# Kernel optimization log

Hardware: AMD Instinct MI355X
Metric: run time of the kernel (lower is better)

## Reference

```python
import jax, jax.numpy as jnp
import numpy as np

B, CIN, CNECK, COUT = 8, 128, 128, 256
NV, NF = 10242, 20480  # icosphere level 5: nv = 10*4^5+2, nf = 20*4^5
EPS = 1e-5


def spmatmul(x, rows, cols, vals, m):
    # x: [..., N]; out[..., r] += vals[k] * x[..., cols[k]] for rows[k] == r
    g = x[..., cols] * vals
    return jnp.zeros(x.shape[:-1] + (m,), x.dtype).at[..., rows].add(g)


def conv1x1(x, w, b):
    # x: [B, Cin, N], w: [Cout, Cin], b: [Cout]
    return jnp.einsum('oi,bin->bon', w, x) + b[None, :, None]


def batchnorm1d(x, gamma, beta):
    # training-mode BN over (batch, spatial) per channel, biased variance
    mean = jnp.mean(x, axis=(0, 2), keepdims=True)
    var = jnp.var(x, axis=(0, 2), keepdims=True)
    xhat = (x - mean) * jax.lax.rsqrt(var + EPS)
    return gamma[None, :, None] * xhat + beta[None, :, None]


def setup_inputs() -> dict:
    key = jax.random.key(0)
    ks = jax.random.split(key, 16)

    def coo(k, nrows, per_row, ncols, scale):
        rows = jnp.repeat(jnp.arange(nrows, dtype=jnp.int32), per_row)
        cols = jax.random.randint(k, (nrows * per_row,), 0, ncols, dtype=jnp.int32)
        vals = jax.random.normal(jax.random.fold_in(k, 1), (nrows * per_row,), jnp.float32) * scale
        return rows, cols, vals

    Gr, Gc, Gv = coo(ks[0], 3 * NF, 3, NV, 0.5)
    Lr, Lc, Lv = coo(ks[1], NV, 7, NV, 0.3)
    Fr, Fc, Fv = coo(ks[2], NV, 6, NF, 1.0 / 6.0)

    def nrm(k, shape, scale=1.0):
        return jax.random.normal(k, shape, jnp.float32) * scale

    s_in = 1.0 / np.sqrt(CIN)
    s_nk = 1.0 / np.sqrt(CNECK)
    s_cf = 1.0 / np.sqrt(4 * CNECK)
    return {
        'x': nrm(ks[3], (B, CIN, NV)),
        'w1a': nrm(ks[4], (CNECK, CIN), s_in), 'b1a': nrm(ks[5], (CNECK,), s_in),
        'g1a': jnp.ones((CNECK,), jnp.float32), 'be1a': jnp.zeros((CNECK,), jnp.float32),
        'coeffs': nrm(ks[6], (CNECK * 4, CNECK), s_cf),
        'g2a': jnp.ones((CNECK,), jnp.float32), 'be2a': jnp.zeros((CNECK,), jnp.float32),
        'w3a': nrm(ks[7], (COUT, CNECK), s_nk), 'b3a': nrm(ks[8], (COUT,), s_nk),
        'g3a': jnp.ones((COUT,), jnp.float32), 'be3a': jnp.zeros((COUT,), jnp.float32),
        'w1b': nrm(ks[9], (COUT, CIN), s_in), 'b1b': nrm(ks[10], (COUT,), s_in),
        'g1b': jnp.ones((COUT,), jnp.float32), 'be1b': jnp.zeros((COUT,), jnp.float32),
        'G_vals': Gv, 'L_vals': Lv, 'F2V_vals': Fv,
        'EW': nrm(ks[11], (NF, 3)), 'NS': nrm(ks[12], (NF, 3)),
        'G_rows': Gr, 'G_cols': Gc,
        'L_rows': Lr, 'L_cols': Lc,
        'F2V_rows': Fr, 'F2V_cols': Fc,
    }


def mesh_conv(h, coeffs, G_rows, G_cols, G_vals, L_rows, L_cols, L_vals,
              F2V_rows, F2V_cols, F2V_vals, EW, NS):
    b, c, nv = h.shape
    # gradient on faces: [B,C,3*NF] -> [B,C,3,NF] -> [B,C,NF,3]
    grad_face = spmatmul(h, G_rows, G_cols, G_vals, 3 * NF)
    grad_face = grad_face.reshape(b, c, 3, NF).transpose(0, 1, 3, 2)
    laplacian = spmatmul(h, L_rows, L_cols, L_vals, NV)
    identity = h  # stride=1 => nv_prev == nv
    gf_ew = jnp.sum(grad_face * EW, axis=-1)  # [B,C,NF]
    gf_ns = jnp.sum(grad_face * NS, axis=-1)
    gv_ew = spmatmul(gf_ew, F2V_rows, F2V_cols, F2V_vals, NV)
    gv_ns = spmatmul(gf_ns, F2V_rows, F2V_cols, F2V_vals, NV)
    feat = jnp.stack([identity, laplacian, gv_ew, gv_ns], axis=-1)  # [B,C,NV,4]
    # [B,NV,C*4] @ [C*4,Cout] -> [B,Cout,NV]  (note: no bias added in original forward)
    out = jnp.matmul(feat.transpose(0, 2, 1, 3).reshape(b, nv, c * 4), coeffs)
    return out.transpose(0, 2, 1)


def reference(x, w1a, b1a, g1a, be1a, coeffs, g2a, be2a, w3a, b3a, g3a, be3a,
              w1b, b1b, g1b, be1b, G_vals, L_vals, F2V_vals, EW, NS,
              G_rows, G_cols, L_rows, L_cols, F2V_rows, F2V_cols):
    # shortcut branch: conv_1b -> bn_1b
    x2 = batchnorm1d(conv1x1(x, w1b, b1b), g1b, be1b)
    # main branch
    h = jax.nn.relu(batchnorm1d(conv1x1(x, w1a, b1a), g1a, be1a))
    h = mesh_conv(h, coeffs, G_rows, G_cols, G_vals, L_rows, L_cols, L_vals,
                  F2V_rows, F2V_cols, F2V_vals, EW, NS)
    h = jax.nn.relu(batchnorm1d(h, g2a, be2a))
    x1 = batchnorm1d(conv1x1(h, w3a, b3a), g3a, be3a)
    return jax.nn.relu(x1 + x2)
```

## Files before the change

### kernel.cpp

```cpp
#include <hip/hip_runtime.h>
#include <math.h>

#define BB   8
#define NVV  10242
#define NFF  20480
#define EPSBN 1e-5f
#define GRAM_BLOCKS 644

typedef __attribute__((ext_vector_type(8))) short bf16x8_t;
typedef __attribute__((ext_vector_type(4))) float f32x4_t;

__device__ inline float bf2f(ushort u) {
    union { uint i; float f; } v; v.i = ((uint)u) << 16; return v.f;
}
__device__ inline ushort f2bf(float f) {
    union { float f; uint i; } v; v.f = f;
    const uint r = v.i + 0x7fffu + ((v.i >> 16) & 1u);
    return (ushort)(r >> 16);
}
__device__ inline void unpack2(uint w, float& lo, float& hi) {
    union { uint i; float f; } a, b;
    a.i = w << 16; b.i = w & 0xffff0000u;
    lo = a.f; hi = b.f;
}
__device__ inline uint pack2(float lo, float hi) {
    return (uint)f2bf(lo) | ((uint)f2bf(hi) << 16);
}
__device__ inline void fma8(const uint4 hv, const float w, float s[8]) {
    float lo, hi;
    unpack2(hv.x, lo, hi); s[0] = fmaf(w, lo, s[0]); s[1] = fmaf(w, hi, s[1]);
    unpack2(hv.y, lo, hi); s[2] = fmaf(w, lo, s[2]); s[3] = fmaf(w, hi, s[3]);
    unpack2(hv.z, lo, hi); s[4] = fmaf(w, lo, s[4]); s[5] = fmaf(w, hi, s[5]);
    unpack2(hv.w, lo, hi); s[6] = fmaf(w, lo, s[6]); s[7] = fmaf(w, hi, s[7]);
}
__device__ inline uint4 pack8(const float s[8]) {
    uint4 p;
    p.x = pack2(s[0], s[1]); p.y = pack2(s[2], s[3]);
    p.z = pack2(s[4], s[5]); p.w = pack2(s[6], s[7]);
    return p;
}

__global__ __launch_bounds__(256)
void gram_kernel(const float* __restrict__ x, float* __restrict__ gramPart,
                 float* __restrict__ xsumPart, uint* __restrict__ xTu)
{
    __shared__ __align__(16) ushort Ahi[128 * 64];
    __shared__ __align__(16) ushort Alo[128 * 64];
    const int t = threadIdx.x;
    const int l = t & 63, wid = t >> 6;
    const int l15 = l & 15, l4 = l >> 4;
    f32x4_t acc[2][8];
#pragma unroll
    for (int m = 0; m < 2; ++m)
#pragma unroll
        for (int n = 0; n < 8; ++n) acc[m][n] = (f32x4_t){0.f, 0.f, 0.f, 0.f};
    float xs[8] = {0.f, 0.f, 0.f, 0.f, 0.f, 0.f, 0.f, 0.f};

    for (int s = 0; s < 2; ++s) {
        const int cc = blockIdx.x * 2 + s;
        const int b = cc / 161, tb = cc % 161, v0 = tb * 64;
#pragma unroll
        for (int i = 0; i < 8; ++i) {
            const int item = t + (i << 8);
            const int c = item >> 4, vq = item & 15;
            const int gv = v0 + (vq << 2);
            const float* xp = x + ((size_t)b * 128 + c) * NVV + gv;
            float4 xv = make_float4(0.f, 0.f, 0.f, 0.f);
            if (gv + 4 <= NVV) {
                xv = *reinterpret_cast<const float4*>(xp);
            } else {
                if (gv     < NVV) xv.x = xp[0];
                if (gv + 1 < NVV) xv.y = xp[1];
            }
            xs[i] += xv.x + xv.y + xv.z + xv.w;
            const ushort h0 = f2bf(xv.x), h1 = f2bf(xv.y), h2 = f2bf(xv.z), h3 = f2bf(xv.w);
            const ushort e0 = f2bf(xv.x - bf2f(h0)), e1 = f2bf(xv.y - bf2f(h1));
            const ushort e2 = f2bf(xv.z - bf2f(h2)), e3 = f2bf(xv.w - bf2f(h3));
            uint2 hp, lp;
            hp.x = (uint)h0 | ((uint)h1 << 16); hp.y = (uint)h2 | ((uint)h3 << 16);
            lp.x = (uint)e0 | ((uint)e1 << 16); lp.y = (uint)e2 | ((uint)e3 << 16);
            const int byte = (c << 7) + (vq << 3);
            const int swz = byte ^ ((c & 7) << 4);
            *reinterpret_cast<uint2*>((char*)Ahi + swz) = hp;
            *reinterpret_cast<uint2*>((char*)Alo + swz) = lp;
        }
        __syncthreads();
        {
            const int v = t & 63, cq = t >> 6;
            const int gv = v0 + v;
            if (gv < NVV) {
                uint4* rowp = reinterpret_cast<uint4*>(xTu + ((size_t)b * NVV + gv) * 64) + (cq << 2);
#pragma unroll
                for (int k2 = 0; k2 < 4; ++k2) {
                    uint wrd[4];
#pragma unroll
                    for (int w2 = 0; w2 < 4; ++w2) {
                        const int c0 = (cq << 5) + (k2 << 3) + (w2 << 1);
                        const int b0 = ((c0) << 7) + (v << 1);
                        const int b1 = ((c0 + 1) << 7) + (v << 1);
                        const ushort q0 = *reinterpret_cast<const ushort*>((const char*)Ahi + (b0 ^ ((c0 & 7) << 4)));
                        const ushort q1 = *reinterpret_cast<const ushort*>((const char*)Ahi + (b1 ^ (((c0 + 1) & 7) << 4)));
                        wrd[w2] = (uint)q0 | ((uint)q1 << 16);
                    }
                    rowp[k2] = make_uint4(wrd[0], wrd[1], wrd[2], wrd[3]);
                }
            }
        }
#pragma unroll
        for (int kk2 = 0; kk2 < 2; ++kk2) {
            bf16x8_t ah[2], al[2];
#pragma unroll
            for (int m = 0; m < 2; ++m) {
                const int row = wid * 32 + m * 16 + l15;
                const int byte = (row << 7) + (kk2 << 6) + (l4 << 4);
                ah[m] = *reinterpret_cast<const bf16x8_t*>((const char*)Ahi + (byte ^ ((row & 7) << 4)));
                al[m] = *reinterpret_cast<const bf16x8_t*>((const char*)Alo + (byte ^ ((row & 7) << 4)));
            }
#pragma unroll
            for (int n = 0; n < 8; ++n) {
                const int rn = n * 16 + l15;
                const int byte = (rn << 7) + (kk2 << 6) + (l4 << 4);
                const bf16x8_t bh = *reinterpret_cast<const bf16x8_t*>((const char*)Ahi + (byte ^ ((rn & 7) << 4)));
                const bf16x8_t bl = *reinterpret_cast<const bf16x8_t*>((const char*)Alo + (byte ^ ((rn & 7) << 4)));
#pragma unroll
                for (int m = 0; m < 2; ++m) {
                    acc[m][n] = __builtin_amdgcn_mfma_f32_16x16x32_bf16(ah[m], bh, acc[m][n], 0, 0, 0);
                    acc[m][n] = __builtin_amdgcn_mfma_f32_16x16x32_bf16(ah[m], bl, acc[m][n], 0, 0, 0);
                    acc[m][n] = __builtin_amdgcn_mfma_f32_16x16x32_bf16(al[m], bh, acc[m][n], 0, 0, 0);
                }
            }
        }
        __syncthreads();
    }
    float* gp = gramPart + (size_t)blockIdx.x * 16384;
#pragma unroll
    for (int m = 0; m < 2; ++m)
#pragma unroll
        for (int n = 0; n < 8; ++n)
#pragma unroll
            for (int j = 0; j < 4; ++j) {
                const int row = wid * 32 + m * 16 + l4 * 4 + j;
                const int col = n * 16 + l15;
                gp[row * 128 + col] = acc[m][n][j];
            }
#pragma unroll
    for (int i = 0; i < 8; ++i) {
        xs[i] += __shfl_xor(xs[i], 1);
        xs[i] += __shfl_xor(xs[i], 2);
        xs[i] += __shfl_xor(xs[i], 4);
        xs[i] += __shfl_xor(xs[i], 8);
    }
    if ((l & 15) == 0) {
#pragma unroll
        for (int i = 0; i < 8; ++i)
            xsumPart[(size_t)blockIdx.x * 128 + wid * 4 + l4 + i * 16] = xs[i];
    }
}

__global__ void reduce_gram_kernel(const float* __restrict__ gp, const float* __restrict__ xp,
                                   float* __restrict__ Gram, float* __restrict__ xsum)
{
    const int tid = blockIdx.x * 256 + threadIdx.x;
    for (int e = tid; e < 16384; e += 64 * 256) {
        float s = 0.f;
        for (int i = 0; i < GRAM_BLOCKS; ++i) s += gp[(size_t)i * 16384 + e];
        Gram[e] = s;
    }
    if (blockIdx.x == 0 && threadIdx.x < 128) {
        float s = 0.f;
        for (int i = 0; i < GRAM_BLOCKS; ++i) s += xp[(size_t)i * 128 + threadIdx.x];
        xsum[threadIdx.x] = s;
    }
}

__global__ __launch_bounds__(128)
void stats_ab_kernel(const float* __restrict__ Gram, const float* __restrict__ xsum,
                     const float* __restrict__ w1a, const float* __restrict__ g1a,
                     const float* __restrict__ be1a,
                     const float* __restrict__ w1b, const float* __restrict__ g1b,
                     const float* __restrict__ be1b,
                     float* __restrict__ alpha_a, float* __restrict__ beta_a,
                     float* __restrict__ alpha_b, float* __restrict__ beta_b)
{
    const int t = threadIdx.x;
    const int cc = blockIdx.x;
    const float invN = 1.f / (float)(BB * NVV);
    const bool isA = cc < 128;
    const int c = isA ? cc : cc - 128;
    const float* Wrow = isA ? (w1a + (size_t)c * 128) : (w1b + (size_t)c * 128);
    __shared__ float Wr[128];
    __shared__ float red[4];
    Wr[t] = Wrow[t];
    __syncthreads();
    float gi = 0.f;
    const float* Grow = Gram + (size_t)t * 128;
    for (int j = 0; j < 128; ++j) gi = fmaf(Grow[j], Wr[j], gi);
    float pi = Wr[t] * gi * invN;
    float qi = (xsum[t] * invN) * Wr[t];
    for (int off = 32; off > 0; off >>= 1) {
        pi += __shfl_down(pi, off);
        qi += __shfl_down(qi, off);
    }
    const int wid = t >> 6;
    if ((t & 63) == 0) { red[wid] = pi; red[2 + wid] = qi; }
    __syncthreads();
    if (t == 0) {
        const float P = red[0] + red[1], Q = red[2] + red[3];
        const float var = P - Q * Q;
        const float g = isA ? g1a[c] : g1b[c];
        const float be = isA ? be1a[c] : be1b[c];
        const float a = g * rsqrtf(var + EPSBN);
        if (isA) { alpha_a[c] = a; beta_a[c] = be - a * Q; }
        else     { alpha_b[c] = a; beta_b[c] = be - a * Q; }
    }
}

__global__ __launch_bounds__(256)
void prepack_weights_kernel(const float* __restrict__ w1a, const float* __restrict__ w1b,
                            const float* __restrict__ w3a, uint* __restrict__ wpk)
{
    const int j = blockIdx.x * 256 + threadIdx.x;
    const int seg = j >> 12;
    const int slab = seg >> 1, kc = (seg & 1) << 6;
    const int u = j & 4095;
    const int o = u >> 5;
    const int inner = (u << 2) & 127;
    const int inner0 = inner ^ ((o & 7) << 4);
    const int kp = inner0 >> 2;
    const float* W;
    if (slab == 0)      W = w1a;
    else if (slab <= 2) W = w1b + (size_t)(slab - 1) * 128 * 128;
    else                W = w3a + (size_t)(slab - 3) * 128 * 128;
    const float2 wv = *reinterpret_cast<const float2*>(&W[(size_t)o * 128 + kc + 2 * kp]);
    wpk[j] = pack2(wv.x, wv.y);
}

template <int MODE>
__global__ __launch_bounds__(256)
void mfma_conv_kernel(const ushort* __restrict__ Asrc, const uint4* __restrict__ wpk,
                      const float* __restrict__ aIn, const float* __restrict__ bIn,
                      const float* __restrict__ aA, const float* __restrict__ bA,
                      const float* __restrict__ aB, const float* __restrict__ bB,
                      ushort* __restrict__ hOut, ushort* __restrict__ x2Out,
                      ushort* __restrict__ x1Out,
                      float* __restrict__ statSum, float* __restrict__ statSsq)
{
    __shared__ __align__(16) ushort As[128 * 128];
    __shared__ __align__(16) ushort Bs[128 * 64];
    __shared__ float statS[256], statQ[256];
    const int t = threadIdx.x;
    const int bid = blockIdx.x;
    const int b = bid & 7, vblk = bid >> 3;
    const int v0 = vblk * 128;
    const int l = t & 63, wid = t >> 6;
    const int wr = wid >> 1, wc = wid & 1;
    const int l15 = l & 15, l4 = l >> 4;

#pragma unroll
    for (int i = 0; i < 8; ++i) {
        const int item = t + (i << 8);
        const int r = item >> 4, piece = item & 15;
        const int cb = piece * 8;
        const int v = v0 + r;
        uint4 pk = make_uint4(0u, 0u, 0u, 0u);
        if (v < NVV) {
            pk = *reinterpret_cast<const uint4*>(Asrc + ((size_t)b * NVV + v) * 128 + cb);
            if (MODE == 1) {
                float s[8];
                unpack2(pk.x, s[0], s[1]); unpack2(pk.y, s[2], s[3]);
                unpack2(pk.z, s[4], s[5]); unpack2(pk.w, s[6], s[7]);
                const float4 a0 = *reinterpret_cast<const float4*>(&aIn[cb]);
                const float4 a1 = *reinterpret_cast<const float4*>(&aIn[cb + 4]);
                const float4 b0 = *reinterpret_cast<const float4*>(&bIn[cb]);
                const float4 b1 = *reinterpret_cast<const float4*>(&bIn[cb + 4]);
                s[0] = fmaxf(fmaf(a0.x, s[0], b0.x), 0.f);
                s[1] = fmaxf(fmaf(a0.y, s[1], b0.y), 0.f);
                s[2] = fmaxf(fmaf(a0.z, s[2], b0.z), 0.f);
                s[3] = fmaxf(fmaf(a0.w, s[3], b0.w), 0.f);
                s[4] = fmaxf(fmaf(a1.x, s[4], b1.x), 0.f);
                s[5] = fmaxf(fmaf(a1.y, s[5], b1.y), 0.f);
                s[6] = fmaxf(fmaf(a1.z, s[6], b1.z), 0.f);
                s[7] = fmaxf(fmaf(a1.w, s[7], b1.w), 0.f);
                pk = pack8(s);
            }
        }
        const int byte = (r << 8) + (piece << 4);
        *reinterpret_cast<uint4*>((char*)As + (byte ^ ((r & 7) << 4))) = pk;
    }

    const int NZ = (MODE == 0) ? 3 : 2;
    for (int z = 0; z < NZ; ++z) {
        const int slab = (MODE == 0) ? z : (3 + z);
        f32x4_t acc[4][4];
#pragma unroll
        for (int m = 0; m < 4; ++m)
#pragma unroll
            for (int n = 0; n < 4; ++n) acc[m][n] = (f32x4_t){0.f, 0.f, 0.f, 0.f};

        for (int kc = 0; kc < 128; kc += 64) {
            const uint4* wseg = wpk + (size_t)(slab * 2 + (kc >> 6)) * 1024;
#pragma unroll
            for (int i = 0; i < 4; ++i)
                reinterpret_cast<uint4*>(Bs)[t + (i << 8)] = wseg[t + (i << 8)];
            __syncthreads();
#pragma unroll
            for (int kk2 = 0; kk2 < 2; ++kk2) {
                bf16x8_t af[4], bfr[4];
#pragma unroll
                for (int m = 0; m < 4; ++m) {
                    const int row = wr * 64 + m * 16 + l15;
                    const int byte = (row << 8) + (kc << 1) + (kk2 << 6) + (l4 << 4);
                    af[m] = *reinterpret_cast<const bf16x8_t*>((const char*)As + (byte ^ ((row & 7) << 4)));
                }
#pragma unroll
                for (int n = 0; n < 4; ++n) {
                    const int o = wc * 64 + n * 16 + l15;
                    const int byte = (o << 7) + (kk2 << 6) + (l4 << 4);
                    bfr[n] = *reinterpret_cast<const bf16x8_t*>((const char*)Bs + (byte ^ ((o & 7) << 4)));
                }
#pragma unroll
                for (int m = 0; m < 4; ++m)
#pragma unroll
                    for (int n = 0; n < 4; ++n)
                        acc[m][n] = __builtin_amdgcn_mfma_f32_16x16x32_bf16(af[m], bfr[n], acc[m][n], 0, 0, 0);
            }
            __syncthreads();
        }

        if (MODE == 0 && z == 0) {
            float aO[4], bO[4];
#pragma unroll
            for (int n = 0; n < 4; ++n) {
                const int c = wc * 64 + n * 16 + l15;
                aO[n] = aA[c]; bO[n] = bA[c];
            }
#pragma unroll
            for (int m = 0; m < 4; ++m) {
#pragma unroll
                for (int j = 0; j < 4; ++j) {
                    const int v = v0 + wr * 64 + m * 16 + l4 * 4 + j;
                    if (v < NVV) {
                        ushort* mp = hOut + ((size_t)b * NVV + v) * 128 + wc * 64 + l15;
#pragma unroll
                        for (int n = 0; n < 4; ++n)
                            mp[n * 16] = f2bf(fmaxf(fmaf(aO[n], acc[m][n][j], bO[n]), 0.f));
                    }
                }
            }
        } else if (MODE == 0) {
            float aO[4], bO[4];
#pragma unroll
            for (int n = 0; n < 4; ++n) {
                const int cl = wc * 64 + n * 16 + l15;
                aO[n] = aB[(z - 1) * 128 + cl]; bO[n] = bB[(z - 1) * 128 + cl];
            }
#pragma unroll
            for (int m = 0; m < 4; ++m) {
                const int vbase = v0 + wr * 64 + m * 16 + l4 * 4;
#pragma unroll
                for (int n = 0; n < 4; ++n) {
                    const int cl = wc * 64 + n * 16 + l15;
                    const int ch = (z - 1) * 128 + cl;
                    ushort* p = x2Out + ((size_t)b * 256 + ch) * NVV + vbase;
                    if (vbase + 4 <= NVV) {
                        uint* pu = (uint*)p;
                        pu[0] = pack2(fmaf(aO[n], acc[m][n][0], bO[n]),
                                      fmaf(aO[n], acc[m][n][1], bO[n]));
                        pu[1] = pack2(fmaf(aO[n], acc[m][n][2], bO[n]),
                                      fmaf(aO[n], acc[m][n][3], bO[n]));
                    } else {
#pragma unroll
                        for (int j = 0; j < 4; ++j)
                            if (vbase + j < NVV)
                                p[j] = f2bf(fmaf(aO[n], acc[m][n][j], bO[n]));
                    }
                }
            }
        } else {
            float ss[4] = {0.f, 0.f, 0.f, 0.f}, sq[4] = {0.f, 0.f, 0.f, 0.f};
#pragma unroll
            for (int m = 0; m < 4; ++m) {
                const int vbase = v0 + wr * 64 + m * 16 + l4 * 4;
#pragma unroll
                for (int n = 0; n < 4; ++n) {
                    const int cl = wc * 64 + n * 16 + l15;
                    const int ch = z * 128 + cl;
                    ushort* p = x1Out + ((size_t)b * 256 + ch) * NVV + vbase;
                    if (vbase + 4 <= NVV) {
                        float v0f = acc[m][n][0], v1f = acc[m][n][1];
                        float v2f = acc[m][n][2], v3f = acc[m][n][3];
                        uint* pu = (uint*)p;
                        pu[0] = pack2(v0f, v1f);
                        pu[1] = pack2(v2f, v3f);
                        ss[n] += v0f + v1f + v2f + v3f;
                        sq[n] = fmaf(v0f, v0f, sq[n]); sq[n] = fmaf(v1f, v1f, sq[n]);
                        sq[n] = fmaf(v2f, v2f, sq[n]); sq[n] = fmaf(v3f, v3f, sq[n]);
                    } else {
#pragma unroll
                        for (int j = 0; j < 4; ++j) {
                            if (vbase + j < NVV) {
                                const float val = acc[m][n][j];
                                p[j] = f2bf(val);
                                ss[n] += val;
                                sq[n] = fmaf(val, val, sq[n]);
                            }
                        }
                    }
                }
            }
#pragma unroll
            for (int n = 0; n < 4; ++n) {
                ss[n] += __shfl_xor(ss[n], 16); ss[n] += __shfl_xor(ss[n], 32);
                sq[n] += __shfl_xor(sq[n], 16); sq[n] += __shfl_xor(sq[n], 32);
            }
            if (l < 16) {
#pragma unroll
                for (int n = 0; n < 4; ++n) {
                    statS[wr * 128 + wc * 64 + n * 16 + l] = ss[n];
                    statQ[wr * 128 + wc * 64 + n * 16 + l] = sq[n];
                }
            }
            __syncthreads();
            if (t < 128) {
                const int slot = b * 81 + vblk;
                statSum[((size_t)z * 648 + slot) * 128 + t] = statS[t] + statS[128 + t];
                statSsq[((size_t)z * 648 + slot) * 128 + t] = statQ[t] + statQ[128 + t];
            }
            __syncthreads();
        }
    }
}

__global__ __launch_bounds__(256)
void face_kernel(const ushort* __restrict__ h, const float* __restrict__ Gv,
                 const int* __restrict__ Gc, const float* __restrict__ EW,
                 const float* __restrict__ NSm, ushort* __restrict__ gf)
{
    const int t = threadIdx.x;
    const int lane = t & 63, wid = t >> 6;
    const int bid = blockIdx.x;
    const int b = bid & 7;
    const int f = (bid >> 3) * 4 + wid;
    const uint* hb = (const uint*)h + (size_t)b * NVV * 64;
    float ewx = 0.f, ewy = 0.f, nsx = 0.f, nsy = 0.f;
#pragma unroll
    for (int e = 0; e < 3; ++e) {
        const size_t r3 = ((size_t)e * NFF + f) * 3;
        float gx = 0.f, gy = 0.f;
#pragma unroll
        for (int j = 0; j < 3; ++j) {
            const float w = Gv[r3 + j];
            const int col = Gc[r3 + j];
            const uint hv = hb[(size_t)col * 64 + lane];
            float lo, hi; unpack2(hv, lo, hi);
            gx = fmaf(w, lo, gx); gy = fmaf(w, hi, gy);
        }
        const float we = EW[f * 3 + e], wn = NSm[f * 3 + e];
        ewx = fmaf(we, gx, ewx); ewy = fmaf(we, gy, ewy);
        nsx = fmaf(wn, gx, nsx); nsy = fmaf(wn, gy, nsy);
    }
    uint* go = (uint*)gf + ((size_t)b * NFF + f) * 128;
    go[lane]      = pack2(ewx, ewy);
    go[64 + lane] = pack2(nsx, nsy);
}

__global__ __launch_bounds__(256)
void prepack_coeffs_kernel(const float* __restrict__ coeffs, uint* __restrict__ cpk)
{
    const int j = blockIdx.x * 256 + threadIdx.x;
    const int chunk = j >> 12, u = j & 4095;
    const int o = u >> 5;
    const int inner = (u << 2) & 127;
    const int inner0 = inner ^ ((o & 7) << 4);
    const int p = inner0 >> 2;
    const int q = chunk >> 1, c0 = (chunk & 1) << 6;
    const int row0 = (c0 + 2 * p) * 4 + q;
    cpk[j] = pack2(coeffs[(size_t)row0 * 128 + o], coeffs[(size_t)(row0 + 4) * 128 + o]);
}

__global__ __launch_bounds__(512)
void mesh_gemm_kernel(const ushort* __restrict__ h, const ushort* __restrict__ gf,
                      const uint4* __restrict__ cpk,
                      const float* __restrict__ Lv, const int* __restrict__ Lc,
                      const float* __restrict__ Fv, const int* __restrict__ Fc,
                      ushort* __restrict__ meshraw,
                      float* __restrict__ msum, float* __restrict__ mssq)
{
    __shared__ __align__(16) ushort As[128 * 64];
    __shared__ __align__(16) ushort Bs[128 * 64];
    __shared__ float statS[512], statQ[512];
    __shared__ int   LciS[896];
    __shared__ float LwS[896];
    __shared__ int   FciS[768];
    __shared__ float FwS[768];
    const int t = threadIdx.x;
    const int bid = blockIdx.x;
    const int b = bid & 7;
    const int vblk = bid >> 3;
    const int v0 = vblk * 128;
    const int l = t & 63, wid = t >> 6;
    const int wr = wid >> 1, wc = wid & 1;
    const int l15 = l & 15, l4 = l >> 4;
    const size_t hb = (size_t)b * NVV * 128;

    for (int i = t; i < 896; i += 512) {
        const int g = v0 * 7 + i;
        if (g < NVV * 7) { LciS[i] = Lc[g]; LwS[i] = Lv[g]; }
    }
    for (int i = t; i < 768; i += 512) {
        const int g = v0 * 6 + i;
        if (g < NVV * 6) { FciS[i] = Fc[g]; FwS[i] = Fv[g]; }
    }
    __syncthreads();

    f32x4_t acc[2][4];
#pragma unroll
    for (int m = 0; m < 2; ++m)
#pragma unroll
        for (int n = 0; n < 4; ++n) acc[m][n] = (f32x4_t){0.f, 0.f, 0.f, 0.f};

    for (int chunk = 0; chunk < 8; ++chunk) {
        const int q = chunk >> 1, c0 = (chunk & 1) << 6;
#pragma unroll
        for (int i = 0; i < 2; ++i) {
            const int item = t + (i << 9);
            const int r = item >> 3, piece = item & 7;
            const int cb = c0 + piece * 8;
            const int v = v0 + r;
            uint4 pk = make_uint4(0u, 0u, 0u, 0u);
            if (v < NVV) {
                if (q == 0) {
                    pk = *reinterpret_cast<const uint4*>(h + hb + (size_t)v * 128 + cb);
                } else if (q == 1) {
                    float s[8] = {0.f, 0.f, 0.f, 0.f, 0.f, 0.f, 0.f, 0.f};
#pragma unroll
                    for (int j = 0; j < 7; ++j) {
                        const float w = LwS[r * 7 + j];
                        const int col = LciS[r * 7 + j];
                        const uint4 hv = *reinterpret_cast<const uint4*>(h + hb + (size_t)col * 128 + cb);
                        fma8(hv, w, s);
                    }
                    pk = pack8(s);
                } else {
                    const int slab = q - 2;
                    float s[8] = {0.f, 0.f, 0.f, 0.f, 0.f, 0.f, 0.f, 0.f};
#pragma unroll
                    for (int j = 0; j < 6; ++j) {
                        const float w = FwS[r * 6 + j];
                        const int f = FciS[r * 6 + j];
                        const uint4 gv = *reinterpret_cast<const uint4*>(
                            gf + (((size_t)b * NFF + f) * 2 + slab) * 128 + cb);
                        fma8(gv, w, s);
                    }
                    pk = pack8(s);
                }
            }
            const int byte = (r << 7) + (piece << 4);
            *reinterpret_cast<uint4*>((char*)As + (byte ^ ((r & 7) << 4))) = pk;
        }
#pragma unroll
        for (int i = 0; i < 2; ++i) {
            const int idx = t + (i << 9);
            reinterpret_cast<uint4*>(Bs)[idx] = cpk[chunk * 1024 + idx];
        }
        __syncthreads();
#pragma unroll
        for (int kk2 = 0; kk2 < 2; ++kk2) {
            bf16x8_t af[2], bfr[4];
#pragma unroll
            for (int m = 0; m < 2; ++m) {
                const int row = wr * 32 + m * 16 + l15;
                const int byte = (row << 7) + (kk2 << 6) + (l4 << 4);
                af[m] = *reinterpret_cast<const bf16x8_t*>((const char*)As + (byte ^ ((row & 7) << 4)));
            }
#pragma unroll
            for (int n = 0; n < 4; ++n) {
                const int o = wc * 64 + n * 16 + l15;
                const int byte = (o << 7) + (kk2 << 6) + (l4 << 4);
                bfr[n] = *reinterpret_cast<const bf16x8_t*>((const char*)Bs + (byte ^ ((o & 7) << 4)));
            }
#pragma unroll
            for (int m = 0; m < 2; ++m)
#pragma unroll
                for (int n = 0; n < 4; ++n)
                    acc[m][n] = __builtin_amdgcn_mfma_f32_16x16x32_bf16(af[m], bfr[n], acc[m][n], 0, 0, 0);
        }
        __syncthreads();
    }
    float ss[4] = {0.f, 0.f, 0.f, 0.f}, sq[4] = {0.f, 0.f, 0.f, 0.f};
#pragma unroll
    for (int m = 0; m < 2; ++m) {
#pragma unroll
        for (int j = 0; j < 4; ++j) {
            const int row = wr * 32 + m * 16 + l4 * 4 + j;
            const int v = v0 + row;
            if (v < NVV) {
                ushort* mp = meshraw + hb + (size_t)v * 128 + wc * 64 + l15;
#pragma unroll
                for (int n = 0; n < 4; ++n) {
                    const float val = acc[m][n][j];
                    mp[n * 16] = f2bf(val);
                    ss[n] += val;
                    sq[n] = fmaf(val, val, sq[n]);
                }
            }
        }
    }
#pragma unroll
    for (int n = 0; n < 4; ++n) {
        ss[n] += __shfl_xor(ss[n], 16); ss[n] += __shfl_xor(ss[n], 32);
        sq[n] += __shfl_xor(sq[n], 16); sq[n] += __shfl_xor(sq[n], 32);
    }
    if (l < 16) {
#pragma unroll
        for (int n = 0; n < 4; ++n) {
            statS[wr * 128 + wc * 64 + n * 16 + l] = ss[n];
            statQ[wr * 128 + wc * 64 + n * 16 + l] = sq[n];
        }
    }
    __syncthreads();
    if (t < 128) {
        const int blk = b * 81 + vblk;
        msum[(size_t)blk * 128 + t] = statS[t] + statS[128 + t] + statS[256 + t] + statS[384 + t];
        mssq[(size_t)blk * 128 + t] = statQ[t] + statQ[128 + t] + statQ[256 + t] + statQ[384 + t];
    }
}

__global__ __launch_bounds__(256)
void finalize_stats_kernel(const float* __restrict__ s, const float* __restrict__ q, int count,
                           const float* __restrict__ g, const float* __restrict__ be,
                           float* __restrict__ alpha, float* __restrict__ beta, int split)
{
    const int c = blockIdx.x, t = threadIdx.x;
    const size_t base = split ? ((size_t)(c >> 7) * count * 128 + (c & 127)) : (size_t)c;
    float ls = 0.f, lq = 0.f;
    for (int i = t; i < count; i += 256) {
        ls += s[base + (size_t)i * 128];
        lq += q[base + (size_t)i * 128];
    }
    __shared__ float rs[256], rq[256];
    rs[t] = ls; rq[t] = lq;
    __syncthreads();
    for (int off = 128; off > 0; off >>= 1) {
        if (t < off) { rs[t] += rs[t + off]; rq[t] += rq[t + off]; }
        __syncthreads();
    }
    if (t == 0) {
        const float invN = 1.f / (float)(BB * NVV);
        const float mean = rs[0] * invN;
        const float var = rq[0] * invN - mean * mean;
        const float a = g[c] * rsqrtf(var + EPSBN);
        alpha[c] = a;
        beta[c] = be[c] - a * mean;
    }
}

__global__ __launch_bounds__(256)
void final_kernel(float* __restrict__ out, const ushort* __restrict__ x1,
                  const ushort* __restrict__ x2,
                  const float* __restrict__ alpha3, const float* __restrict__ beta3)
{
    const int blk = blockIdx.x;
    const int o = blk & 255;
    const float a = alpha3[o], bb = beta3[o];
    float2* po = reinterpret_cast<float2*>(out + (size_t)blk * NVV);
    const uint* p1 = reinterpret_cast<const uint*>(x1 + (size_t)blk * NVV);
    const uint* p2 = reinterpret_cast<const uint*>(x2 + (size_t)blk * NVV);
    for (int i = threadIdx.x; i < NVV / 2; i += 256) {
        float a1, b1, a2, b2;
        unpack2(p1[i], a1, b1);
        unpack2(p2[i], a2, b2);
        po[i] = make_float2(fmaxf(fmaf(a, a1, bb) + a2, 0.f),
                            fmaxf(fmaf(a, b1, bb) + b2, 0.f));
    }
}

extern "C" void kernel_launch(void* const* d_in, const int* in_sizes, int n_in,
                              void* d_out, int out_size, void* d_ws, size_t ws_size,
                              hipStream_t stream)
{
    (void)in_sizes; (void)n_in; (void)out_size;
    const float* x      = (const float*)d_in[0];
    const float* w1a    = (const float*)d_in[1];
    const float* g1a    = (const float*)d_in[3];
    const float* be1a   = (const float*)d_in[4];
    const float* coeffs = (const float*)d_in[5];
    const float* g2a    = (const float*)d_in[6];
    const float* be2a   = (const float*)d_in[7];
    const float* w3a    = (const float*)d_in[8];
    const float* g3a    = (const float*)d_in[10];
    const float* be3a   = (const float*)d_in[11];
    const float* w1b    = (const float*)d_in[12];
    const float* g1b    = (const float*)d_in[14];
    const float* be1b   = (const float*)d_in[15];
    const float* Gv     = (const float*)d_in[16];
    const float* Lv     = (const float*)d_in[17];
    const float* Fv     = (const float*)d_in[18];
    const float* EW     = (const float*)d_in[19];
    const float* NSm    = (const float*)d_in[20];
    const int*   Gc     = (const int*)d_in[22];
    const int*   Lc     = (const int*)d_in[24];
    const int*   Fc     = (const int*)d_in[26];

    char* base = (char*)d_ws;
    size_t off = 0;
    auto alloc = [&](size_t bytes) { char* p = base + off; off += (bytes + 255) & ~(size_t)255; return p; };

    const size_t gfBytes = (size_t)BB * NFF * 2 * 128 * 2;
    char* region0   = alloc(gfBytes);
    float* gramPart = (float*)region0;
    float* xsumPart = (float*)(region0 + (size_t)GRAM_BLOCKS * 16384 * 4);
    ushort* gf      = (ushort*)region0;
    ushort* x1      = (ushort*)region0;

    ushort* xT      = (ushort*)alloc((size_t)BB * NVV * 128 * 2);
    ushort* h       = (ushort*)alloc((size_t)BB * NVV * 128 * 2);
    ushort* meshraw = (ushort*)alloc((size_t)BB * NVV * 128 * 2);
    ushort* x2      = (ushort*)alloc((size_t)BB * 256 * NVV * 2);
    uint*  cpk      = (uint*)alloc(32768 * 4);
    uint*  wpk      = (uint*)alloc(40960 * 4);
    float* Gram     = (float*)alloc(16384 * 4);
    float* xsum     = (float*)alloc(128 * 4);
    float* alpha_a  = (float*)alloc(128 * 4);
    float* beta_a   = (float*)alloc(128 * 4);
    float* alpha_b  = (float*)alloc(256 * 4);
    float* beta_b   = (float*)alloc(256 * 4);
    float* alpha2   = (float*)alloc(128 * 4);
    float* beta2    = (float*)alloc(128 * 4);
    float* alpha3   = (float*)alloc(256 * 4);
    float* beta3    = (float*)alloc(256 * 4);
    float* msum     = (float*)alloc((size_t)648 * 128 * 4);
    float* mssq     = (float*)alloc((size_t)648 * 128 * 4);
    float* x1sum    = (float*)alloc((size_t)2 * 648 * 128 * 4);
    float* x1ssq    = (float*)alloc((size_t)2 * 648 * 128 * 4);
    if (off > ws_size) return;

    gram_kernel<<<GRAM_BLOCKS, 256, 0, stream>>>(x, gramPart, xsumPart, (uint*)xT);
    reduce_gram_kernel<<<64, 256, 0, stream>>>(gramPart, xsumPart, Gram, xsum);
    stats_ab_kernel<<<384, 128, 0, stream>>>(Gram, xsum, w1a, g1a, be1a, w1b, g1b, be1b,
                                             alpha_a, beta_a, alpha_b, beta_b);
    prepack_coeffs_kernel<<<128, 256, 0, stream>>>(coeffs, cpk);
    prepack_weights_kernel<<<160, 256, 0, stream>>>(w1a, w1b, w3a, wpk);
    mfma_conv_kernel<0><<<648, 256, 0, stream>>>(
        xT, (const uint4*)wpk, nullptr, nullptr, alpha_a, beta_a, alpha_b, beta_b,
        h, x2, nullptr, nullptr, nullptr);
    face_kernel<<<(NFF / 4) * 8, 256, 0, stream>>>(h, Gv, Gc, EW, NSm, gf);
    mesh_gemm_kernel<<<648, 512, 0, stream>>>(h, gf, (const uint4*)cpk,
                                              Lv, Lc, Fv, Fc, meshraw, msum, mssq);
    finalize_stats_kernel<<<128, 256, 0, stream>>>(msum, mssq, 648, g2a, be2a, alpha2, beta2, 0);
    mfma_conv_kernel<1><<<648, 256, 0, stream>>>(
        meshraw, (const uint4*)wpk, alpha2, beta2, nullptr, nullptr, nullptr, nullptr,
        nullptr, nullptr, x1, x1sum, x1ssq);
    finalize_stats_kernel<<<256, 256, 0, stream>>>(x1sum, x1ssq, 648, g3a, be3a, alpha3, beta3, 1);
    final_kernel<<<2048, 256, 0, stream>>>((float*)d_out, x1, x2, alpha3, beta3);
}
```

Before: 316.7 us.

## Halve vertex tile to 64 rows in conv and mesh GEMM kernels

The MFMA conv and mesh GEMM kernels now process 64 vertices per block instead of 128, so the grid doubles to 1288 blocks. The mesh GEMM drops from 512 to 256 threads. Each wave now owns a 16-row strip across all 128 output channels (8 accumulators) rather than a 2D sub-tile. The intent is more blocks for the 256 CUs and a smaller LDS footprint for higher occupancy, at the cost of reloading the B weight tiles twice as often and writing more partial BN stats. Stats buffers and the finalize counts are resized to match.

```diff
diff --git a/kernel.cpp b/kernel.cpp
--- a/kernel.cpp
+++ b/kernel.cpp
@@ -235,6 +235,20 @@
     wpk[j] = pack2(wv.x, wv.y);
 }
 
+__global__ __launch_bounds__(256)
+void prepack_coeffs_kernel(const float* __restrict__ coeffs, uint* __restrict__ cpk)
+{
+    const int j = blockIdx.x * 256 + threadIdx.x;
+    const int chunk = j >> 12, u = j & 4095;
+    const int o = u >> 5;
+    const int inner = (u << 2) & 127;
+    const int inner0 = inner ^ ((o & 7) << 4);
+    const int p = inner0 >> 2;
+    const int q = chunk >> 1, c0 = (chunk & 1) << 6;
+    const int row0 = (c0 + 2 * p) * 4 + q;
+    cpk[j] = pack2(coeffs[(size_t)row0 * 128 + o], coeffs[(size_t)(row0 + 4) * 128 + o]);
+}
+
 template <int MODE>
 __global__ __launch_bounds__(256)
 void mfma_conv_kernel(const ushort* __restrict__ Asrc, const uint4* __restrict__ wpk,
@@ -245,19 +259,18 @@
                       ushort* __restrict__ x1Out,
                       float* __restrict__ statSum, float* __restrict__ statSsq)
 {
-    __shared__ __align__(16) ushort As[128 * 128];
+    __shared__ __align__(16) ushort As[64 * 128];
     __shared__ __align__(16) ushort Bs[128 * 64];
-    __shared__ float statS[256], statQ[256];
+    __shared__ float statS[512], statQ[512];
     const int t = threadIdx.x;
     const int bid = blockIdx.x;
     const int b = bid & 7, vblk = bid >> 3;
-    const int v0 = vblk * 128;
+    const int v0 = vblk * 64;
     const int l = t & 63, wid = t >> 6;
-    const int wr = wid >> 1, wc = wid & 1;
     const int l15 = l & 15, l4 = l >> 4;
 
 #pragma unroll
-    for (int i = 0; i < 8; ++i) {
+    for (int i = 0; i < 4; ++i) {
         const int item = t + (i << 8);
         const int r = item >> 4, piece = item & 15;
         const int cb = piece * 8;
@@ -291,11 +304,9 @@
     const int NZ = (MODE == 0) ? 3 : 2;
     for (int z = 0; z < NZ; ++z) {
         const int slab = (MODE == 0) ? z : (3 + z);
-        f32x4_t acc[4][4];
-#pragma unroll
-        for (int m = 0; m < 4; ++m)
-#pragma unroll
-            for (int n = 0; n < 4; ++n) acc[m][n] = (f32x4_t){0.f, 0.f, 0.f, 0.f};
+        f32x4_t acc[8];
+#pragma unroll
+        for (int n = 0; n < 8; ++n) acc[n] = (f32x4_t){0.f, 0.f, 0.f, 0.f};
 
         for (int kc = 0; kc < 128; kc += 64) {
             const uint4* wseg = wpk + (size_t)(slab * 2 + (kc >> 6)) * 1024;
@@ -305,126 +316,115 @@
             __syncthreads();
 #pragma unroll
             for (int kk2 = 0; kk2 < 2; ++kk2) {
-                bf16x8_t af[4], bfr[4];
-#pragma unroll
-                for (int m = 0; m < 4; ++m) {
-                    const int row = wr * 64 + m * 16 + l15;
-                    const int byte = (row << 8) + (kc << 1) + (kk2 << 6) + (l4 << 4);
-                    af[m] = *reinterpret_cast<const bf16x8_t*>((const char*)As + (byte ^ ((row & 7) << 4)));
+                const int row = wid * 16 + l15;
+                const int abyte = (row << 8) + (kc << 1) + (kk2 << 6) + (l4 << 4);
+                const bf16x8_t af = *reinterpret_cast<const bf16x8_t*>(
+                    (const char*)As + (abyte ^ ((row & 7) << 4)));
+#pragma unroll
+                for (int n = 0; n < 8; ++n) {
+                    const int o = n * 16 + l15;
+                    const int bbyte = (o << 7) + (kk2 << 6) + (l4 << 4);
+                    const bf16x8_t bfr = *reinterpret_cast<const bf16x8_t*>(
+                        (const char*)Bs + (bbyte ^ ((o & 7) << 4)));
+                    acc[n] = __builtin_amdgcn_mfma_f32_16x16x32_bf16(af, bfr, acc[n], 0, 0, 0);
                 }
-#pragma unroll
-                for (int n = 0; n < 4; ++n) {
-                    const int o = wc * 64 + n * 16 + l15;
-                    const int byte = (o << 7) + (kk2 << 6) + (l4 << 4);
-                    bfr[n] = *reinterpret_cast<const bf16x8_t*>((const char*)Bs + (byte ^ ((o & 7) << 4)));
+            }
+            __syncthreads();
+        }
+
+        if (MODE == 0 && z == 0) {
+            float aO[8], bO[8];
+#pragma unroll
+            for (int n = 0; n < 8; ++n) {
+                const int c = n * 16 + l15;
+                aO[n] = aA[c]; bO[n] = bA[c];
+            }
+#pragma unroll
+            for (int j = 0; j < 4; ++j) {
+                const int v = v0 + wid * 16 + l4 * 4 + j;
+                if (v < NVV) {
+                    ushort* mp = hOut + ((size_t)b * NVV + v) * 128 + l15;
+#pragma unroll
+                    for (int n = 0; n < 8; ++n)
+                        mp[n * 16] = f2bf(fmaxf(fmaf(aO[n], acc[n][j], bO[n]), 0.f));
                 }
-#pragma unroll
-                for (int m = 0; m < 4; ++m)
-#pragma unroll
-                    for (int n = 0; n < 4; ++n)
-                        acc[m][n] = __builtin_amdgcn_mfma_f32_16x16x32_bf16(af[m], bfr[n], acc[m][n], 0, 0, 0);
-            }
-            __syncthreads();
-        }
-
-        if (MODE == 0 && z == 0) {
-            float aO[4], bO[4];
-#pragma unroll
-            for (int n = 0; n < 4; ++n) {
-                const int c = wc * 64 + n * 16 + l15;
-                aO[n] = aA[c]; bO[n] = bA[c];
-            }
-#pragma unroll
-            for (int m = 0; m < 4; ++m) {
-#pragma unroll
-                for (int j = 0; j < 4; ++j) {
-                    const int v = v0 + wr * 64 + m * 16 + l4 * 4 + j;
-                    if (v < NVV) {
-                        ushort* mp = hOut + ((size_t)b * NVV + v) * 128 + wc * 64 + l15;
-#pragma unroll
-                        for (int n = 0; n < 4; ++n)
-                            mp[n * 16] = f2bf(fmaxf(fmaf(aO[n], acc[m][n][j], bO[n]), 0.f));
-                    }
+            }
+        } else if (MODE == 0) {
+            float aO[8], bO[8];
+#pragma unroll
+            for (int n = 0; n < 8; ++n) {
+                const int cl = n * 16 + l15;
+                aO[n] = aB[(z - 1) * 128 + cl]; bO[n] = bB[(z - 1) * 128 + cl];
+            }
+            const int vbase = v0 + wid * 16 + l4 * 4;
+#pragma unroll
+            for (int n = 0; n < 8; ++n) {
+                const int cl = n * 16 + l15;
+                const int ch = (z - 1) * 128 + cl;
+                ushort* p = x2Out + ((size_t)b * 256 + ch) * NVV + vbase;
+                if (vbase + 4 <= NVV) {
+                    uint* pu = (uint*)p;
+                    pu[0] = pack2(fmaf(aO[n], acc[n][0], bO[n]),
+                                  fmaf(aO[n], acc[n][1], bO[n]));
+                    pu[1] = pack2(fmaf(aO[n], acc[n][2], bO[n]),
+                                  fmaf(aO[n], acc[n][3], bO[n]));
+                } else {
+#pragma unroll
+                    for (int j = 0; j < 4; ++j)
+                        if (vbase + j < NVV)
+                            p[j] = f2bf(fmaf(aO[n], acc[n][j], bO[n]));
                 }
             }
-        } else if (MODE == 0) {
-            float aO[4], bO[4];
-#pragma unroll
-            for (int n = 0; n < 4; ++n) {
-                const int cl = wc * 64 + n * 16 + l15;
-                aO[n] = aB[(z - 1) * 128 + cl]; bO[n] = bB[(z - 1) * 128 + cl];
-            }
-#pragma unroll
-            for (int m = 0; m < 4; ++m) {
-                const int vbase = v0 + wr * 64 + m * 16 + l4 * 4;
-#pragma unroll
-                for (int n = 0; n < 4; ++n) {
-                    const int cl = wc * 64 + n * 16 + l15;
-                    const int ch = (z - 1) * 128 + cl;
-                    ushort* p = x2Out + ((size_t)b * 256 + ch) * NVV + vbase;
-                    if (vbase + 4 <= NVV) {
-                        uint* pu = (uint*)p;
-                        pu[0] = pack2(fmaf(aO[n], acc[m][n][0], bO[n]),
-                                      fmaf(aO[n], acc[m][n][1], bO[n]));
-                        pu[1] = pack2(fmaf(aO[n], acc[m][n][2], bO[n]),
-                                      fmaf(aO[n], acc[m][n][3], bO[n]));
-                    } else {
-#pragma unroll
-                        for (int j = 0; j < 4; ++j)
-                            if (vbase + j < NVV)
-                                p[j] = f2bf(fmaf(aO[n], acc[m][n][j], bO[n]));
-                    }
-                }
-            }
         } else {
-            float ss[4] = {0.f, 0.f, 0.f, 0.f}, sq[4] = {0.f, 0.f, 0.f, 0.f};
-#pragma unroll
-            for (int m = 0; m < 4; ++m) {
-                const int vbase = v0 + wr * 64 + m * 16 + l4 * 4;
-#pragma unroll
-                for (int n = 0; n < 4; ++n) {
-                    const int cl = wc * 64 + n * 16 + l15;
-                    const int ch = z * 128 + cl;
-                    ushort* p = x1Out + ((size_t)b * 256 + ch) * NVV + vbase;
-                    if (vbase + 4 <= NVV) {
-                        float v0f = acc[m][n][0], v1f = acc[m][n][1];
-                        float v2f = acc[m][n][2], v3f = acc[m][n][3];
-                        uint* pu = (uint*)p;
-                        pu[0] = pack2(v0f, v1f);
-                        pu[1] = pack2(v2f, v3f);
-                        ss[n] += v0f + v1f + v2f + v3f;
-                        sq[n] = fmaf(v0f, v0f, sq[n]); sq[n] = fmaf(v1f, v1f, sq[n]);
-                        sq[n] = fmaf(v2f, v2f, sq[n]); sq[n] = fmaf(v3f, v3f, sq[n]);
-                    } else {
-#pragma unroll
-                        for (int j = 0; j < 4; ++j) {
-                            if (vbase + j < NVV) {
-                                const float val = acc[m][n][j];
-                                p[j] = f2bf(val);
-                                ss[n] += val;
-                                sq[n] = fmaf(val, val, sq[n]);
-                            }
+            float ss[8], sq[8];
+#pragma unroll
+            for (int n = 0; n < 8; ++n) { ss[n] = 0.f; sq[n] = 0.f; }
+            const int vbase = v0 + wid * 16 + l4 * 4;
+#pragma unroll
+            for (int n = 0; n < 8; ++n) {
+                const int cl = n * 16 + l15;
+                const int ch = z * 128 + cl;
+                ushort* p = x1Out + ((size_t)b * 256 + ch) * NVV + vbase;
+                if (vbase + 4 <= NVV) {
+                    float v0f = acc[n][0], v1f = acc[n][1];
+                    float v2f = acc[n][2], v3f = acc[n][3];
+                    uint* pu = (uint*)p;
+                    pu[0] = pack2(v0f, v1f);
+                    pu[1] = pack2(v2f, v3f);
+                    ss[n] += v0f + v1f + v2f + v3f;
+                    sq[n] = fmaf(v0f, v0f, sq[n]); sq[n] = fmaf(v1f, v1f, sq[n]);
+                    sq[n] = fmaf(v2f, v2f, sq[n]); sq[n] = fmaf(v3f, v3f, sq[n]);
+                } else {
+#pragma unroll
+                    for (int j = 0; j < 4; ++j) {
+                        if (vbase + j < NVV) {
+                            const float val = acc[n][j];
+                            p[j] = f2bf(val);
+                            ss[n] += val;
+                            sq[n] = fmaf(val, val, sq[n]);
                         }
                     }
                 }
             }
 #pragma unroll
-            for (int n = 0; n < 4; ++n) {
+            for (int n = 0; n < 8; ++n) {
                 ss[n] += __shfl_xor(ss[n], 16); ss[n] += __shfl_xor(ss[n], 32);
                 sq[n] += __shfl_xor(sq[n], 16); sq[n] += __shfl_xor(sq[n], 32);
             }
             if (l < 16) {
 #pragma unroll
-                for (int n = 0; n < 4; ++n) {
-                    statS[wr * 128 + wc * 64 + n * 16 + l] = ss[n];
-                    statQ[wr * 128 + wc * 64 + n * 16 + l] = sq[n];
+                for (int n = 0; n < 8; ++n) {
+                    statS[wid * 128 + n * 16 + l] = ss[n];
+                    statQ[wid * 128 + n * 16 + l] = sq[n];
                 }
             }
             __syncthreads();
             if (t < 128) {
-                const int slot = b * 81 + vblk;
-                statSum[((size_t)z * 648 + slot) * 128 + t] = statS[t] + statS[128 + t];
-                statSsq[((size_t)z * 648 + slot) * 128 + t] = statQ[t] + statQ[128 + t];
+                const int slot = b * 161 + vblk;
+                statSum[((size_t)z * 1288 + slot) * 128 + t] =
+                    statS[t] + statS[128 + t] + statS[256 + t] + statS[384 + t];
+                statSsq[((size_t)z * 1288 + slot) * 128 + t] =
+                    statQ[t] + statQ[128 + t] + statQ[256 + t] + statQ[384 + t];
             }
             __syncthreads();
         }
@@ -465,20 +465,6 @@
 }
 
 __global__ __launch_bounds__(256)
-void prepack_coeffs_kernel(const float* __restrict__ coeffs, uint* __restrict__ cpk)
-{
-    const int j = blockIdx.x * 256 + threadIdx.x;
-    const int chunk = j >> 12, u = j & 4095;
-    const int o = u >> 5;
-    const int inner = (u << 2) & 127;
-    const int inner0 = inner ^ ((o & 7) << 4);
-    const int p = inner0 >> 2;
-    const int q = chunk >> 1, c0 = (chunk & 1) << 6;
-    const int row0 = (c0 + 2 * p) * 4 + q;
-    cpk[j] = pack2(coeffs[(size_t)row0 * 128 + o], coeffs[(size_t)(row0 + 4) * 128 + o]);
-}
-
-__global__ __launch_bounds__(512)
 void mesh_gemm_kernel(const ushort* __restrict__ h, const ushort* __restrict__ gf,
                       const uint4* __restrict__ cpk,
                       const float* __restrict__ Lv, const int* __restrict__ Lc,
@@ -486,44 +472,41 @@
                       ushort* __restrict__ meshraw,
                       float* __restrict__ msum, float* __restrict__ mssq)
 {
-    __shared__ __align__(16) ushort As[128 * 64];
+    __shared__ __align__(16) ushort As[64 * 64];
     __shared__ __align__(16) ushort Bs[128 * 64];
     __shared__ float statS[512], statQ[512];
-    __shared__ int   LciS[896];
-    __shared__ float LwS[896];
-    __shared__ int   FciS[768];
-    __shared__ float FwS[768];
+    __shared__ int   LciS[448];
+    __shared__ float LwS[448];
+    __shared__ int   FciS[384];
+    __shared__ float FwS[384];
     const int t = threadIdx.x;
     const int bid = blockIdx.x;
     const int b = bid & 7;
     const int vblk = bid >> 3;
-    const int v0 = vblk * 128;
+    const int v0 = vblk * 64;
     const int l = t & 63, wid = t >> 6;
-    const int wr = wid >> 1, wc = wid & 1;
     const int l15 = l & 15, l4 = l >> 4;
     const size_t hb = (size_t)b * NVV * 128;
 
-    for (int i = t; i < 896; i += 512) {
+    for (int i = t; i < 448; i += 256) {
         const int g = v0 * 7 + i;
         if (g < NVV * 7) { LciS[i] = Lc[g]; LwS[i] = Lv[g]; }
     }
-    for (int i = t; i < 768; i += 512) {
+    for (int i = t; i < 384; i += 256) {
         const int g = v0 * 6 + i;
         if (g < NVV * 6) { FciS[i] = Fc[g]; FwS[i] = Fv[g]; }
     }
     __syncthreads();
 
-    f32x4_t acc[2][4];
-#pragma unroll
-    for (int m = 0; m < 2; ++m)
-#pragma unroll
-        for (int n = 0; n < 4; ++n) acc[m][n] = (f32x4_t){0.f, 0.f, 0.f, 0.f};
+    f32x4_t acc[8];
+#pragma unroll
+    for (int n = 0; n < 8; ++n) acc[n] = (f32x4_t){0.f, 0.f, 0.f, 0.f};
 
     for (int chunk = 0; chunk < 8; ++chunk) {
         const int q = chunk >> 1, c0 = (chunk & 1) << 6;
 #pragma unroll
         for (int i = 0; i < 2; ++i) {
-            const int item = t + (i << 9);
+            const int item = t + (i << 8);
             const int r = item >> 3, piece = item & 7;
             const int cb = c0 + piece * 8;
             const int v = v0 + r;
@@ -559,68 +542,61 @@
             *reinterpret_cast<uint4*>((char*)As + (byte ^ ((r & 7) << 4))) = pk;
         }
 #pragma unroll
-        for (int i = 0; i < 2; ++i) {
-            const int idx = t + (i << 9);
+        for (int i = 0; i < 4; ++i) {
+            const int idx = t + (i << 8);
             reinterpret_cast<uint4*>(Bs)[idx] = cpk[chunk * 1024 + idx];
         }
         __syncthreads();
 #pragma unroll
         for (int kk2 = 0; kk2 < 2; ++kk2) {
-            bf16x8_t af[2], bfr[4];
-#pragma unroll
-            for (int m = 0; m < 2; ++m) {
-                const int row = wr * 32 + m * 16 + l15;
-                const int byte = (row << 7) + (kk2 << 6) + (l4 << 4);
-                af[m] = *reinterpret_cast<const bf16x8_t*>((const char*)As + (byte ^ ((row & 7) << 4)));
-            }
-#pragma unroll
-            for (int n = 0; n < 4; ++n) {
-                const int o = wc * 64 + n * 16 + l15;
-                const int byte = (o << 7) + (kk2 << 6) + (l4 << 4);
-                bfr[n] = *reinterpret_cast<const bf16x8_t*>((const char*)Bs + (byte ^ ((o & 7) << 4)));
-            }
-#pragma unroll
-            for (int m = 0; m < 2; ++m)
-#pragma unroll
-                for (int n = 0; n < 4; ++n)
-                    acc[m][n] = __builtin_amdgcn_mfma_f32_16x16x32_bf16(af[m], bfr[n], acc[m][n], 0, 0, 0);
+            const int row = wid * 16 + l15;
+            const int abyte = (row << 7) + (kk2 << 6) + (l4 << 4);
+            const bf16x8_t af = *reinterpret_cast<const bf16x8_t*>(
+                (const char*)As + (abyte ^ ((row & 7) << 4)));
+#pragma unroll
+            for (int n = 0; n < 8; ++n) {
+                const int o = n * 16 + l15;
+                const int bbyte = (o << 7) + (kk2 << 6) + (l4 << 4);
+                const bf16x8_t bfr = *reinterpret_cast<const bf16x8_t*>(
+                    (const char*)Bs + (bbyte ^ ((o & 7) << 4)));
+                acc[n] = __builtin_amdgcn_mfma_f32_16x16x32_bf16(af, bfr, acc[n], 0, 0, 0);
+            }
         }
         __syncthreads();
     }
-    float ss[4] = {0.f, 0.f, 0.f, 0.f}, sq[4] = {0.f, 0.f, 0.f, 0.f};
-#pragma unroll
-    for (int m = 0; m < 2; ++m) {
-#pragma unroll
-        for (int j = 0; j < 4; ++j) {
-            const int row = wr * 32 + m * 16 + l4 * 4 + j;
-            const int v = v0 + row;
-            if (v < NVV) {
-                ushort* mp = meshraw + hb + (size_t)v * 128 + wc * 64 + l15;
-#pragma unroll
-                for (int n = 0; n < 4; ++n) {
-                    const float val = acc[m][n][j];
-                    mp[n * 16] = f2bf(val);
-                    ss[n] += val;
-                    sq[n] = fmaf(val, val, sq[n]);
-                }
-            }
-        }
-    }
-#pragma unroll
-    for (int n = 0; n < 4; ++n) {
+    float ss[8], sq[8];
+#pragma unroll
+    for (int n = 0; n < 8; ++n) { ss[n] = 0.f; sq[n] = 0.f; }
+#pragma unroll
+    for (int j = 0; j < 4; ++j) {
+        const int row = wid * 16 + l4 * 4 + j;
+        const int v = v0 + row;
+        if (v < NVV) {
+            ushort* mp = meshraw + hb + (size_t)v * 128 + l15;
+#pragma unroll
+            for (int n = 0; n < 8; ++n) {
+                const float val = acc[n][j];
+                mp[n * 16] = f2bf(val);
+                ss[n] += val;
+                sq[n] = fmaf(val, val, sq[n]);
+            }
+        }
+    }
+#pragma unroll
+    for (int n = 0; n < 8; ++n) {
         ss[n] += __shfl_xor(ss[n], 16); ss[n] += __shfl_xor(ss[n], 32);
         sq[n] += __shfl_xor(sq[n], 16); sq[n] += __shfl_xor(sq[n], 32);
     }
     if (l < 16) {
 #pragma unroll
-        for (int n = 0; n < 4; ++n) {
-            statS[wr * 128 + wc * 64 + n * 16 + l] = ss[n];
-            statQ[wr * 128 + wc * 64 + n * 16 + l] = sq[n];
+        for (int n = 0; n < 8; ++n) {
+            statS[wid * 128 + n * 16 + l] = ss[n];
+            statQ[wid * 128 + n * 16 + l] = sq[n];
         }
     }
     __syncthreads();
     if (t < 128) {
-        const int blk = b * 81 + vblk;
+        const int blk = b * 161 + vblk;
         msum[(size_t)blk * 128 + t] = statS[t] + statS[128 + t] + statS[256 + t] + statS[384 + t];
         mssq[(size_t)blk * 128 + t] = statQ[t] + statQ[128 + t] + statQ[256 + t] + statQ[384 + t];
     }
@@ -729,10 +705,10 @@
     float* beta2    = (float*)alloc(128 * 4);
     float* alpha3   = (float*)alloc(256 * 4);
     float* beta3    = (float*)alloc(256 * 4);
-    float* msum     = (float*)alloc((size_t)648 * 128 * 4);
-    float* mssq     = (float*)alloc((size_t)648 * 128 * 4);
-    float* x1sum    = (float*)alloc((size_t)2 * 648 * 128 * 4);
-    float* x1ssq    = (float*)alloc((size_t)2 * 648 * 128 * 4);
+    float* msum     = (float*)alloc((size_t)1288 * 128 * 4);
+    float* mssq     = (float*)alloc((size_t)1288 * 128 * 4);
+    float* x1sum    = (float*)alloc((size_t)2 * 1288 * 128 * 4);
+    float* x1ssq    = (float*)alloc((size_t)2 * 1288 * 128 * 4);
     if (off > ws_size) return;
 
     gram_kernel<<<GRAM_BLOCKS, 256, 0, stream>>>(x, gramPart, xsumPart, (uint*)xT);
@@ -741,16 +717,16 @@
                                              alpha_a, beta_a, alpha_b, beta_b);
     prepack_coeffs_kernel<<<128, 256, 0, stream>>>(coeffs, cpk);
     prepack_weights_kernel<<<160, 256, 0, stream>>>(w1a, w1b, w3a, wpk);
-    mfma_conv_kernel<0><<<648, 256, 0, stream>>>(
+    mfma_conv_kernel<0><<<1288, 256, 0, stream>>>(
         xT, (const uint4*)wpk, nullptr, nullptr, alpha_a, beta_a, alpha_b, beta_b,
         h, x2, nullptr, nullptr, nullptr);
     face_kernel<<<(NFF / 4) * 8, 256, 0, stream>>>(h, Gv, Gc, EW, NSm, gf);
-    mesh_gemm_kernel<<<648, 512, 0, stream>>>(h, gf, (const uint4*)cpk,
-                                              Lv, Lc, Fv, Fc, meshraw, msum, mssq);
-    finalize_stats_kernel<<<128, 256, 0, stream>>>(msum, mssq, 648, g2a, be2a, alpha2, beta2, 0);
-    mfma_conv_kernel<1><<<648, 256, 0, stream>>>(
+    mesh_gemm_kernel<<<1288, 256, 0, stream>>>(h, gf, (const uint4*)cpk,
+                                               Lv, Lc, Fv, Fc, meshraw, msum, mssq);
+    finalize_stats_kernel<<<128, 256, 0, stream>>>(msum, mssq, 1288, g2a, be2a, alpha2, beta2, 0);
+    mfma_conv_kernel<1><<<1288, 256, 0, stream>>>(
         meshraw, (const uint4*)wpk, alpha2, beta2, nullptr, nullptr, nullptr, nullptr,
         nullptr, nullptr, x1, x1sum, x1ssq);
-    finalize_stats_kernel<<<256, 256, 0, stream>>>(x1sum, x1ssq, 648, g3a, be3a, alpha3, beta3, 1);
+    finalize_stats_kernel<<<256, 256, 0, stream>>>(x1sum, x1ssq, 1288, g3a, be3a, alpha3, beta3, 1);
     final_kernel<<<2048, 256, 0, stream>>>((float*)d_out, x1, x2, alpha3, beta3);
 }
```

New measurement: 301.5 us. 1.05x faster.
